# Performance work log

Measured on AMD Instinct MI355X. Metric: run time of the kernel, lower is better.

## Reference

```python
import jax, jax.numpy as jnp
import numpy as np

B, L, D = 4, 2048, 1024   # batch, seq_len, input_channels
S = 4096                  # param_token_num
DV = 1024                 # output_channels


def setup_inputs() -> dict:
    key = jax.random.key(0)
    k1, k2, k3 = jax.random.split(key, 3)
    return {
        "inputs": jax.random.normal(k1, (B, L, D), dtype=jnp.float32),
        "key_param_tokens": jax.random.normal(k2, (S, D), dtype=jnp.float32),
        "value_param_tokens": jax.random.normal(k3, (S, DV), dtype=jnp.float32),
    }


def reference(inputs, key_param_tokens, value_param_tokens):
    # scores: [B, L, S] — full score matrix (this is what a fused kernel would avoid)
    scores = jnp.einsum("bld,sd->bls", inputs, key_param_tokens)
    # gelu_l2_norm: exact (erf) gelu, then L2-normalize over S and rescale by sqrt(S)
    g = jax.nn.gelu(scores, approximate=False)
    l2 = jnp.linalg.norm(g, axis=-1, keepdims=True)
    w = g / l2 * jnp.sqrt(jnp.asarray(g.shape[-1], g.dtype))
    # weighted sum over param value tokens: [B, L, DV]
    return jnp.einsum("bls,sv->blv", w, value_param_tokens)
```

## Files before the change

### kernel.cpp

```cpp
#include <hip/hip_runtime.h>
#include <hip/hip_bf16.h>
#include <stdint.h>

#define M_ROWS 8192
#define D_DIM  1024
#define S_DIM  4096
#define DV_DIM 1024

typedef __attribute__((ext_vector_type(8))) short bf16x8;
typedef __attribute__((ext_vector_type(4))) float f32x4;
typedef unsigned short u16;

static __device__ __forceinline__ u16 f2bf(float x) {
  union { float f; unsigned u; } v; v.f = x;
  unsigned r = v.u + 0x7FFFu + ((v.u >> 16) & 1u);
  return (u16)(r >> 16);
}
static __device__ __forceinline__ float bf2f(u16 h) {
  union { unsigned u; float f; } v; v.u = ((unsigned)h) << 16;
  return v.f;
}
static __device__ __forceinline__ float gelu_fast(float x) {
  float u = 0.7978845608028654f * x * (1.0f + 0.044715f * x * x);
  float e = __expf(2.0f * u);
  float t = 1.0f - 2.0f / (e + 1.0f);
  return 0.5f * x * (1.0f + t);
}

static __device__ __forceinline__ void gload16(const void* g, void* l) {
  __builtin_amdgcn_global_load_lds(
      (__attribute__((address_space(1))) void*)(void*)(g),
      (__attribute__((address_space(3))) void*)(l), 16, 0, 0);
}

__global__ __launch_bounds__(256)
void cast_f32_bf16(const float* __restrict__ in, u16* __restrict__ out, int n4) {
  const int i = blockIdx.x * 256 + threadIdx.x;
  if (i >= n4) return;
  const float4 v = ((const float4*)in)[i];
  ushort4 o;
  o.x = f2bf(v.x); o.y = f2bf(v.y); o.z = f2bf(v.z); o.w = f2bf(v.w);
  ((ushort4*)out)[i] = o;
}

__global__ __launch_bounds__(256)
void transpose_cast(const float* __restrict__ V, u16* __restrict__ VT, int R, int C) {
  __shared__ float tile[32][33];
  const int tx = threadIdx.x & 31;
  const int ty = threadIdx.x >> 5;
  const int r0 = blockIdx.y * 32;
  const int c0 = blockIdx.x * 32;
#pragma unroll
  for (int dy = 0; dy < 32; dy += 8)
    tile[ty + dy][tx] = V[(long)(r0 + ty + dy) * C + (c0 + tx)];
  __syncthreads();
#pragma unroll
  for (int dy = 0; dy < 32; dy += 8)
    VT[(long)(c0 + ty + dy) * R + (r0 + tx)] = f2bf(tile[tx][ty + dy]);
}

__global__ __launch_bounds__(256)
void row_scale(const u16* __restrict__ G, float* __restrict__ scale, int S) {
  const int row = blockIdx.x;
  const u16* g = G + (long)row * S;
  float ssq = 0.f;
  for (int i = threadIdx.x * 8; i < S; i += 256 * 8) {
    bf16x8 v = *(const bf16x8*)&g[i];
#pragma unroll
    for (int j = 0; j < 8; ++j) {
      float f = bf2f((u16)v[j]);
      ssq += f * f;
    }
  }
#pragma unroll
  for (int off = 32; off > 0; off >>= 1)
    ssq += __shfl_down(ssq, off, 64);
  __shared__ float wsum[4];
  if ((threadIdx.x & 63) == 0) wsum[threadIdx.x >> 6] = ssq;
  __syncthreads();
  if (threadIdx.x == 0) {
    float t = wsum[0] + wsum[1] + wsum[2] + wsum[3];
    scale[row] = 64.0f * rsqrtf(t + 1e-30f);
  }
}

__global__ __launch_bounds__(256)
void add_inplace(float* __restrict__ Out, const float* __restrict__ P1, int n4) {
  for (int i = blockIdx.x * 256 + threadIdx.x; i < n4; i += 2048 * 256) {
    float4 a = ((const float4*)Out)[i];
    const float4 b = ((const float4*)P1)[i];
    a.x += b.x; a.y += b.y; a.z += b.z; a.w += b.w;
    ((float4*)Out)[i] = a;
  }
}


#define BARRIER asm volatile("s_barrier" ::: "memory")
#define VM4 asm volatile("s_waitcnt vmcnt(4)" ::: "memory")
#define VM2 asm volatile("s_waitcnt vmcnt(2)" ::: "memory")
#define VM0 asm volatile("s_waitcnt vmcnt(0)" ::: "memory")

#define PHASE(P, STAGES, WAITS)                                               \
  {                                                                           \
    bf16x8 af[2][2];                                                          \
    _Pragma("unroll")                                                         \
    for (int j = 0; j < 2; ++j) {                                             \
      const int ar = wm * 128 + ((P) * 2 + j) * 16 + fr;                      \
      af[j][0] = rdfrag(la, ar, 0);                                           \
      af[j][1] = rdfrag(la, ar, 1);                                           \
    }                                                                         \
    STAGES;                                                                   \
    BARRIER;                                                                  \
    __builtin_amdgcn_s_setprio(1);                                            \
    _Pragma("unroll")                                                         \
    for (int j = 0; j < 2; ++j) {                                             \
      _Pragma("unroll")                                                       \
      for (int n = 0; n < NF; ++n) {                                          \
        acc[(P) * 2 + j][n] = __builtin_amdgcn_mfma_f32_16x16x32_bf16(        \
            af[j][0], bfr[n][0], acc[(P) * 2 + j][n], 0, 0, 0);               \
        acc[(P) * 2 + j][n] = __builtin_amdgcn_mfma_f32_16x16x32_bf16(        \
            af[j][1], bfr[n][1], acc[(P) * 2 + j][n], 0, 0, 0);               \
      }                                                                       \
    }                                                                         \
    __builtin_amdgcn_s_setprio(0);                                            \
    WAITS;                                                                    \
    BARRIER;                                                                  \
  }

#define READ_B                                                                \
  {                                                                           \
    _Pragma("unroll")                                                         \
    for (int n = 0; n < NF; ++n) {                                            \
      const int br = wn * WNT + n * 16 + fr;                                  \
      bfr[n][0] = rdfrag(lb, br, 0);                                          \
      bfr[n][1] = rdfrag(lb, br, 1);                                          \
    }                                                                         \
  }

template <int MODE, int BN, bool SPLITK>
__global__ __launch_bounds__(512, 2)
void gemm8p(const u16* __restrict__ A, const u16* __restrict__ Bm,
            void* __restrict__ Cout0, void* __restrict__ Cout1,
            const float* __restrict__ scale,
            const int K, const int lda, const int ldb,
            const int N, const int nBN, const int nWG) {
  constexpr int BM = 256, BK = 64;
  constexpr int WNT = BN / 4;
  constexpr int NF = WNT / 16;

  __shared__ u16 ldsA[2][BM * BK];
  __shared__ u16 ldsB[2][BN * BK];

  const int tid = threadIdx.x;
  const int lane = tid & 63;
  const int wv = tid >> 6;
  const int wm = wv >> 2, wn = wv & 3;
  const int fr = lane & 15, hi = lane >> 4;

  int wg;
  {
    const int q = nWG >> 3, r = nWG & 7;
    const int x = blockIdx.x & 7, ix = blockIdx.x >> 3;
    wg = (x < r ? x * (q + 1) : r * (q + 1) + (x - r) * q) + ix;
  }
  void* Cout = Cout0;
  if constexpr (SPLITK) {
    const int half = nWG >> 1;
    const int ks = (wg >= half) ? 1 : 0;
    wg -= ks * half;
    A += (long)ks * K;
    Bm += (long)ks * K;
    if (ks) Cout = Cout1;
  }
  const int bm = wg / nBN, bn = wg % nBN;
  const long aR0 = (long)bm * BM;
  const long bR0 = (long)bn * BN;

  const int srow = tid >> 3;
  const int sch = (tid & 7) ^ (srow & 7);
  const long aoff = (aR0 + srow) * (long)lda + sch * 8;
  const long boff = (bR0 + srow) * (long)ldb + sch * 8;

  auto SA = [&](int buf, int r, int kOff) {
    gload16(A + aoff + ((long)r * 64) * lda + kOff, &ldsA[buf][r * 4096 + tid * 8]);
  };
  auto SB = [&](int buf, int r, int kOff) {
    gload16(Bm + boff + ((long)r * 64) * ldb + kOff, &ldsB[buf][r * 4096 + tid * 8]);
  };
  auto rdfrag = [&](const u16* base, int row, int kk) -> bf16x8 {
    return *(const bf16x8*)&base[row * 64 + (((kk << 2) | hi) ^ (row & 7)) * 8];
  };

  f32x4 acc[8][NF];
#pragma unroll
  for (int m = 0; m < 8; ++m)
#pragma unroll
    for (int n = 0; n < NF; ++n)
      acc[m][n] = f32x4{0.f, 0.f, 0.f, 0.f};

  bf16x8 bfr[NF][2];
  const int nK = K / BK;

  if constexpr (BN == 256) {
    SB(0, 0, 0); SB(0, 1, 0); SB(0, 2, 0); SB(0, 3, 0);
  } else {
    SB(0, 0, 0); SB(0, 1, 0);
  }
  SA(0, 0, 0); SA(0, 2, 0); SA(0, 1, 0); SA(0, 3, 0);
  VM2;
  BARRIER;

  int cur = 0;
  for (int kt = 0; kt < nK - 1; ++kt) {
    const int kN = (kt + 1) * BK;
    const int nxt = cur ^ 1;
    const u16* la = ldsA[cur];
    const u16* lb = ldsB[cur];
    READ_B;
    if constexpr (BN == 256) {
      PHASE(0, { SB(nxt, 0, kN); SB(nxt, 1, kN); }, {});
      PHASE(1, { SB(nxt, 2, kN); SB(nxt, 3, kN); }, VM4);
      PHASE(2, { SA(nxt, 0, kN); SA(nxt, 2, kN); }, {});
      PHASE(3, { SA(nxt, 1, kN); SA(nxt, 3, kN); }, VM2);
    } else {
      PHASE(0, { SB(nxt, 0, kN); SB(nxt, 1, kN); }, {});
      PHASE(1, { SA(nxt, 0, kN); SA(nxt, 2, kN); }, VM4);
      PHASE(2, { SA(nxt, 1, kN); SA(nxt, 3, kN); }, {});
      PHASE(3, {}, VM2);
    }
    cur ^= 1;
  }

  {
    const u16* la = ldsA[cur];
    const u16* lb = ldsB[cur];
    READ_B;
    PHASE(0, {}, {});
    PHASE(1, {}, VM0);
    PHASE(2, {}, {});
    PHASE(3, {}, {});
  }

  const long row0 = aR0 + wm * 128;
  const long col0 = bR0 + wn * WNT;
  if constexpr (MODE == 0) {
    u16* Cg = (u16*)Cout;
#pragma unroll
    for (int m = 0; m < 8; ++m) {
#pragma unroll
      for (int i = 0; i < 4; ++i) {
        const long r = row0 + m * 16 + hi * 4 + i;
#pragma unroll
        for (int n = 0; n < NF; ++n)
          Cg[r * N + col0 + n * 16 + fr] = f2bf(gelu_fast(acc[m][n][i]));
      }
    }
  } else {
    float* Cf = (float*)Cout;
#pragma unroll
    for (int m = 0; m < 8; ++m) {
#pragma unroll
      for (int i = 0; i < 4; ++i) {
        const long r = row0 + m * 16 + hi * 4 + i;
        const float s = scale[r];
#pragma unroll
        for (int n = 0; n < NF; ++n)
          Cf[r * N + col0 + n * 16 + fr] = acc[m][n][i] * s;
      }
    }
  }
}

extern "C" void kernel_launch(void* const* d_in, const int* in_sizes, int n_in,
                              void* d_out, int out_size, void* d_ws, size_t ws_size,
                              hipStream_t stream) {
  const float* Qf = (const float*)d_in[0];
  const float* Kf = (const float*)d_in[1];
  const float* Vf = (const float*)d_in[2];
  float* Out = (float*)d_out;

  const int M = M_ROWS, D = D_DIM, S = S_DIM, DV = DV_DIM;

  char* p = (char*)d_ws;
  u16* Qb = (u16*)p;            p += (size_t)M * D * 2;
  u16* Kb = (u16*)p;            p += (size_t)S * D * 2;
  u16* VT = (u16*)p;            p += (size_t)DV * S * 2;
  float* scalebuf = (float*)p;  p += (size_t)M * 4;
  u16* G = (u16*)p;
  const size_t fixed = (size_t)(p - (char*)d_ws);
  const size_t avail = (ws_size > fixed) ? (ws_size - fixed) : 0;

  const size_t bytes_per_row = (size_t)S * 2;
  size_t rows_fit = avail / bytes_per_row;
  int chunk = (int)((rows_fit / 256) * 256);
  if (chunk > M) chunk = M;
  if (chunk < 256) chunk = 256;

  const size_t Gbytes = (size_t)M * S * 2;
  const size_t Pbytes = (size_t)M * DV * 4;
  const bool use_split = (chunk >= M) && (avail >= Gbytes + Pbytes);
  float* P1 = (float*)((char*)G + Gbytes);

  cast_f32_bf16<<<(M * D / 4 + 255) / 256, 256, 0, stream>>>(Qf, Qb, M * D / 4);
  cast_f32_bf16<<<(S * D / 4 + 255) / 256, 256, 0, stream>>>(Kf, Kb, S * D / 4);
  transpose_cast<<<dim3(DV / 32, S / 32), 256, 0, stream>>>(Vf, VT, S, DV);

  const int nBN1 = S / 256;
  const int nBN2 = DV / 128;
  for (int m0 = 0; m0 < M; m0 += chunk) {
    const int rows = (M - m0 < chunk) ? (M - m0) : chunk;
    const int nWG1 = (rows / 256) * nBN1;
    gemm8p<0, 256, false><<<dim3(nWG1), 512, 0, stream>>>(
        Qb + (size_t)m0 * D, Kb, (void*)G, nullptr, nullptr, D, D, D, S, nBN1, nWG1);
    row_scale<<<rows, 256, 0, stream>>>(G, scalebuf, S);
    if (use_split) {
      const int nBNs = DV / 256;
      const int nWGs = 2 * (M / 256) * nBNs;
      gemm8p<1, 256, true><<<dim3(nWGs), 512, 0, stream>>>(
          G, VT, (void*)Out, (void*)P1, scalebuf, S / 2, S, S, DV, nBNs, nWGs);
      add_inplace<<<2048, 256, 0, stream>>>(Out, P1, M * DV / 4);
    } else {
      const int nWG2 = (rows / 256) * nBN2;
      gemm8p<1, 128, false><<<dim3(nWG2), 512, 0, stream>>>(
          G, VT, (void*)(Out + (size_t)m0 * DV), nullptr, scalebuf, S, S, S, DV, nBN2, nWG2);
    }
  }
}
```

Baseline: 191.0 us.

## Replace per-phase barriers with single end-of-iteration wait and barrier

Drops the barriers and partial vmcnt waits between the four MFMA phases of each K iteration. All next-tile global-to-LDS stages are issued up front, interleaved with the first clusters. A single vmcnt(0) wait plus one barrier then closes each iteration. The aim is to cut barrier overhead and let waves run out of step, at the cost of a coarser double-buffer schedule that exposes the full load latency at the end of each iteration.

```diff
diff --git a/kernel.cpp b/kernel.cpp
--- a/kernel.cpp
+++ b/kernel.cpp
@@ -96,11 +96,9 @@
 
 
 #define BARRIER asm volatile("s_barrier" ::: "memory")
-#define VM4 asm volatile("s_waitcnt vmcnt(4)" ::: "memory")
-#define VM2 asm volatile("s_waitcnt vmcnt(2)" ::: "memory")
 #define VM0 asm volatile("s_waitcnt vmcnt(0)" ::: "memory")
 
-#define PHASE(P, STAGES, WAITS)                                               \
+#define CLUSTER(P)                                                            \
   {                                                                           \
     bf16x8 af[2][2];                                                          \
     _Pragma("unroll")                                                         \
@@ -109,8 +107,6 @@
       af[j][0] = rdfrag(la, ar, 0);                                           \
       af[j][1] = rdfrag(la, ar, 1);                                           \
     }                                                                         \
-    STAGES;                                                                   \
-    BARRIER;                                                                  \
     __builtin_amdgcn_s_setprio(1);                                            \
     _Pragma("unroll")                                                         \
     for (int j = 0; j < 2; ++j) {                                             \
@@ -123,8 +119,6 @@
       }                                                                       \
     }                                                                         \
     __builtin_amdgcn_s_setprio(0);                                            \
-    WAITS;                                                                    \
-    BARRIER;                                                                  \
   }
 
 #define READ_B                                                                \
@@ -206,8 +200,8 @@
   } else {
     SB(0, 0, 0); SB(0, 1, 0);
   }
-  SA(0, 0, 0); SA(0, 2, 0); SA(0, 1, 0); SA(0, 3, 0);
-  VM2;
+  SA(0, 0, 0); SA(0, 1, 0); SA(0, 2, 0); SA(0, 3, 0);
+  VM0;
   BARRIER;
 
   int cur = 0;
@@ -218,16 +212,24 @@
     const u16* lb = ldsB[cur];
     READ_B;
     if constexpr (BN == 256) {
-      PHASE(0, { SB(nxt, 0, kN); SB(nxt, 1, kN); }, {});
-      PHASE(1, { SB(nxt, 2, kN); SB(nxt, 3, kN); }, VM4);
-      PHASE(2, { SA(nxt, 0, kN); SA(nxt, 2, kN); }, {});
-      PHASE(3, { SA(nxt, 1, kN); SA(nxt, 3, kN); }, VM2);
+      SB(nxt, 0, kN); SB(nxt, 1, kN); SB(nxt, 2, kN); SB(nxt, 3, kN);
+      SA(nxt, 0, kN); SA(nxt, 2, kN);
+      CLUSTER(0);
+      SA(nxt, 1, kN); SA(nxt, 3, kN);
+      CLUSTER(1);
+      CLUSTER(2);
+      CLUSTER(3);
     } else {
-      PHASE(0, { SB(nxt, 0, kN); SB(nxt, 1, kN); }, {});
-      PHASE(1, { SA(nxt, 0, kN); SA(nxt, 2, kN); }, VM4);
-      PHASE(2, { SA(nxt, 1, kN); SA(nxt, 3, kN); }, {});
-      PHASE(3, {}, VM2);
-    }
+      SB(nxt, 0, kN); SB(nxt, 1, kN);
+      SA(nxt, 0, kN); SA(nxt, 2, kN);
+      CLUSTER(0);
+      SA(nxt, 1, kN); SA(nxt, 3, kN);
+      CLUSTER(1);
+      CLUSTER(2);
+      CLUSTER(3);
+    }
+    VM0;
+    BARRIER;
     cur ^= 1;
   }
 
@@ -235,10 +237,10 @@
     const u16* la = ldsA[cur];
     const u16* lb = ldsB[cur];
     READ_B;
-    PHASE(0, {}, {});
-    PHASE(1, {}, VM0);
-    PHASE(2, {}, {});
-    PHASE(3, {}, {});
+    CLUSTER(0);
+    CLUSTER(1);
+    CLUSTER(2);
+    CLUSTER(3);
   }
 
   const long row0 = aR0 + wm * 128;
```

After: 211.1 us. 10.5% more time.

## Prefetch B tiles two stages ahead, issuing B loads into the current buffer after reads

Applied to the files above, without the earlier changes.

Restructures the GEMM main loop's global-to-LDS prefetch schedule. A is still loaded one K-step ahead, but B is now loaded two K-steps ahead, reusing the current B buffer after its fragments have been read into registers. This adds a peeled second-to-last iteration and changes the vmcnt waits. The aim is to hide global-load latency better. The risk is hazards from overwriting the current LDS buffer, plus more in-flight loads and different wait counts.

```diff
diff --git a/kernel.cpp b/kernel.cpp
--- a/kernel.cpp
+++ b/kernel.cpp
@@ -201,42 +201,58 @@
   bf16x8 bfr[NF][2];
   const int nK = K / BK;
 
+  SA(0, 0, 0); SA(0, 1, 0); SA(0, 2, 0); SA(0, 3, 0);
   if constexpr (BN == 256) {
     SB(0, 0, 0); SB(0, 1, 0); SB(0, 2, 0); SB(0, 3, 0);
+    SB(1, 0, BK); SB(1, 1, BK); SB(1, 2, BK); SB(1, 3, BK);
+    VM4;
   } else {
     SB(0, 0, 0); SB(0, 1, 0);
-  }
-  SA(0, 0, 0); SA(0, 2, 0); SA(0, 1, 0); SA(0, 3, 0);
-  VM2;
+    SB(1, 0, BK); SB(1, 1, BK);
+    VM2;
+  }
   BARRIER;
 
   int cur = 0;
-  for (int kt = 0; kt < nK - 1; ++kt) {
-    const int kN = (kt + 1) * BK;
+  for (int kt = 0; kt < nK - 2; ++kt) {
     const int nxt = cur ^ 1;
+    const int kA = (kt + 1) * BK;
+    const int kB = (kt + 2) * BK;
     const u16* la = ldsA[cur];
     const u16* lb = ldsB[cur];
     READ_B;
     if constexpr (BN == 256) {
-      PHASE(0, { SB(nxt, 0, kN); SB(nxt, 1, kN); }, {});
-      PHASE(1, { SB(nxt, 2, kN); SB(nxt, 3, kN); }, VM4);
-      PHASE(2, { SA(nxt, 0, kN); SA(nxt, 2, kN); }, {});
-      PHASE(3, { SA(nxt, 1, kN); SA(nxt, 3, kN); }, VM2);
+      PHASE(0, { SA(nxt, 0, kA); SA(nxt, 1, kA); SA(nxt, 2, kA); SA(nxt, 3, kA); }, {});
+      PHASE(1, { SB(cur, 0, kB); SB(cur, 1, kB); }, {});
+      PHASE(2, { SB(cur, 2, kB); SB(cur, 3, kB); }, {});
+      PHASE(3, {}, VM4);
     } else {
-      PHASE(0, { SB(nxt, 0, kN); SB(nxt, 1, kN); }, {});
-      PHASE(1, { SA(nxt, 0, kN); SA(nxt, 2, kN); }, VM4);
-      PHASE(2, { SA(nxt, 1, kN); SA(nxt, 3, kN); }, {});
+      PHASE(0, { SA(nxt, 0, kA); SA(nxt, 1, kA); SA(nxt, 2, kA); SA(nxt, 3, kA); }, {});
+      PHASE(1, { SB(cur, 0, kB); }, {});
+      PHASE(2, { SB(cur, 1, kB); }, {});
       PHASE(3, {}, VM2);
     }
     cur ^= 1;
   }
 
+  {
+    const int nxt = cur ^ 1;
+    const int kA = (nK - 1) * BK;
+    const u16* la = ldsA[cur];
+    const u16* lb = ldsB[cur];
+    READ_B;
+    PHASE(0, { SA(nxt, 0, kA); SA(nxt, 1, kA); SA(nxt, 2, kA); SA(nxt, 3, kA); }, {});
+    PHASE(1, {}, {});
+    PHASE(2, {}, {});
+    PHASE(3, {}, VM0);
+    cur ^= 1;
+  }
   {
     const u16* la = ldsA[cur];
     const u16* lb = ldsB[cur];
     READ_B;
     PHASE(0, {}, {});
-    PHASE(1, {}, VM0);
+    PHASE(1, {}, {});
     PHASE(2, {}, {});
     PHASE(3, {}, {});
   }
```

After: 203.9 us. 6.7% more time.

## Replace 8-wave GEMM with 4-wave kernel computing 128x128 per wave

Applied to the files above, without the earlier changes.

The bf16 MFMA GEMM now uses 256 threads (4 waves) per 256x256 tile instead of 512 threads (8 waves), and each wave computes a 128x128 sub-tile with an 8x8 accumulator array. Each wave therefore loads fewer LDS fragments per MFMA, and the staging of global-to-LDS copies and the vmcnt waits are reordered to fit the smaller wave count. The non-split second GEMM also switches from BN=128 to BN=256. In exchange, register pressure rises sharply (256 accumulator floats per lane) and occupancy falls to one block per CU with fewer waves to hide latency.

```diff
diff --git a/kernel.cpp b/kernel.cpp
--- a/kernel.cpp
+++ b/kernel.cpp
@@ -96,9 +96,7 @@
 
 
 #define BARRIER asm volatile("s_barrier" ::: "memory")
-#define VM4 asm volatile("s_waitcnt vmcnt(4)" ::: "memory")
-#define VM2 asm volatile("s_waitcnt vmcnt(2)" ::: "memory")
-#define VM0 asm volatile("s_waitcnt vmcnt(0)" ::: "memory")
+#define VMW(N) asm volatile("s_waitcnt vmcnt(" #N ")" ::: "memory")
 
 #define PHASE(P, STAGES, WAITS)                                               \
   {                                                                           \
@@ -115,7 +113,7 @@
     _Pragma("unroll")                                                         \
     for (int j = 0; j < 2; ++j) {                                             \
       _Pragma("unroll")                                                       \
-      for (int n = 0; n < NF; ++n) {                                          \
+      for (int n = 0; n < 8; ++n) {                                           \
         acc[(P) * 2 + j][n] = __builtin_amdgcn_mfma_f32_16x16x32_bf16(        \
             af[j][0], bfr[n][0], acc[(P) * 2 + j][n], 0, 0, 0);               \
         acc[(P) * 2 + j][n] = __builtin_amdgcn_mfma_f32_16x16x32_bf16(        \
@@ -130,23 +128,21 @@
 #define READ_B                                                                \
   {                                                                           \
     _Pragma("unroll")                                                         \
-    for (int n = 0; n < NF; ++n) {                                            \
-      const int br = wn * WNT + n * 16 + fr;                                  \
+    for (int n = 0; n < 8; ++n) {                                             \
+      const int br = wn * 128 + n * 16 + fr;                                  \
       bfr[n][0] = rdfrag(lb, br, 0);                                          \
       bfr[n][1] = rdfrag(lb, br, 1);                                          \
     }                                                                         \
   }
 
-template <int MODE, int BN, bool SPLITK>
-__global__ __launch_bounds__(512, 2)
-void gemm8p(const u16* __restrict__ A, const u16* __restrict__ Bm,
+template <int MODE, bool SPLITK>
+__global__ __launch_bounds__(256, 1)
+void gemm4f(const u16* __restrict__ A, const u16* __restrict__ Bm,
             void* __restrict__ Cout0, void* __restrict__ Cout1,
             const float* __restrict__ scale,
             const int K, const int lda, const int ldb,
             const int N, const int nBN, const int nWG) {
-  constexpr int BM = 256, BK = 64;
-  constexpr int WNT = BN / 4;
-  constexpr int NF = WNT / 16;
+  constexpr int BM = 256, BN = 256, BK = 64;
 
   __shared__ u16 ldsA[2][BM * BK];
   __shared__ u16 ldsB[2][BN * BK];
@@ -154,7 +150,7 @@
   const int tid = threadIdx.x;
   const int lane = tid & 63;
   const int wv = tid >> 6;
-  const int wm = wv >> 2, wn = wv & 3;
+  const int wm = wv >> 1, wn = wv & 1;
   const int fr = lane & 15, hi = lane >> 4;
 
   int wg;
@@ -182,32 +178,30 @@
   const long boff = (bR0 + srow) * (long)ldb + sch * 8;
 
   auto SA = [&](int buf, int r, int kOff) {
-    gload16(A + aoff + ((long)r * 64) * lda + kOff, &ldsA[buf][r * 4096 + tid * 8]);
+    gload16(A + aoff + ((long)r * 32) * lda + kOff, &ldsA[buf][r * 2048 + tid * 8]);
   };
   auto SB = [&](int buf, int r, int kOff) {
-    gload16(Bm + boff + ((long)r * 64) * ldb + kOff, &ldsB[buf][r * 4096 + tid * 8]);
+    gload16(Bm + boff + ((long)r * 32) * ldb + kOff, &ldsB[buf][r * 2048 + tid * 8]);
   };
   auto rdfrag = [&](const u16* base, int row, int kk) -> bf16x8 {
     return *(const bf16x8*)&base[row * 64 + (((kk << 2) | hi) ^ (row & 7)) * 8];
   };
 
-  f32x4 acc[8][NF];
+  f32x4 acc[8][8];
 #pragma unroll
   for (int m = 0; m < 8; ++m)
 #pragma unroll
-    for (int n = 0; n < NF; ++n)
+    for (int n = 0; n < 8; ++n)
       acc[m][n] = f32x4{0.f, 0.f, 0.f, 0.f};
 
-  bf16x8 bfr[NF][2];
+  bf16x8 bfr[8][2];
   const int nK = K / BK;
 
-  if constexpr (BN == 256) {
-    SB(0, 0, 0); SB(0, 1, 0); SB(0, 2, 0); SB(0, 3, 0);
-  } else {
-    SB(0, 0, 0); SB(0, 1, 0);
-  }
-  SA(0, 0, 0); SA(0, 2, 0); SA(0, 1, 0); SA(0, 3, 0);
-  VM2;
+  SB(0, 0, 0); SB(0, 1, 0); SB(0, 2, 0); SB(0, 3, 0);
+  SB(0, 4, 0); SB(0, 5, 0); SB(0, 6, 0); SB(0, 7, 0);
+  SA(0, 0, 0); SA(0, 4, 0); SA(0, 1, 0); SA(0, 5, 0);
+  SA(0, 2, 0); SA(0, 6, 0); SA(0, 3, 0); SA(0, 7, 0);
+  VMW(4);
   BARRIER;
 
   int cur = 0;
@@ -217,17 +211,10 @@
     const u16* la = ldsA[cur];
     const u16* lb = ldsB[cur];
     READ_B;
-    if constexpr (BN == 256) {
-      PHASE(0, { SB(nxt, 0, kN); SB(nxt, 1, kN); }, {});
-      PHASE(1, { SB(nxt, 2, kN); SB(nxt, 3, kN); }, VM4);
-      PHASE(2, { SA(nxt, 0, kN); SA(nxt, 2, kN); }, {});
-      PHASE(3, { SA(nxt, 1, kN); SA(nxt, 3, kN); }, VM2);
-    } else {
-      PHASE(0, { SB(nxt, 0, kN); SB(nxt, 1, kN); }, {});
-      PHASE(1, { SA(nxt, 0, kN); SA(nxt, 2, kN); }, VM4);
-      PHASE(2, { SA(nxt, 1, kN); SA(nxt, 3, kN); }, {});
-      PHASE(3, {}, VM2);
-    }
+    PHASE(0, { SB(nxt, 0, kN); SB(nxt, 1, kN); SB(nxt, 2, kN); SB(nxt, 3, kN); }, {});
+    PHASE(1, { SB(nxt, 4, kN); SB(nxt, 5, kN); SB(nxt, 6, kN); SB(nxt, 7, kN); }, VMW(10));
+    PHASE(2, { SA(nxt, 0, kN); SA(nxt, 4, kN); SA(nxt, 1, kN); SA(nxt, 5, kN); }, VMW(8));
+    PHASE(3, { SA(nxt, 2, kN); SA(nxt, 6, kN); SA(nxt, 3, kN); SA(nxt, 7, kN); }, VMW(4));
     cur ^= 1;
   }
 
@@ -236,13 +223,13 @@
     const u16* lb = ldsB[cur];
     READ_B;
     PHASE(0, {}, {});
-    PHASE(1, {}, VM0);
+    PHASE(1, {}, VMW(0));
     PHASE(2, {}, {});
     PHASE(3, {}, {});
   }
 
   const long row0 = aR0 + wm * 128;
-  const long col0 = bR0 + wn * WNT;
+  const long col0 = bR0 + wn * 128;
   if constexpr (MODE == 0) {
     u16* Cg = (u16*)Cout;
 #pragma unroll
@@ -251,7 +238,7 @@
       for (int i = 0; i < 4; ++i) {
         const long r = row0 + m * 16 + hi * 4 + i;
 #pragma unroll
-        for (int n = 0; n < NF; ++n)
+        for (int n = 0; n < 8; ++n)
           Cg[r * N + col0 + n * 16 + fr] = f2bf(gelu_fast(acc[m][n][i]));
       }
     }
@@ -264,7 +251,7 @@
         const long r = row0 + m * 16 + hi * 4 + i;
         const float s = scale[r];
 #pragma unroll
-        for (int n = 0; n < NF; ++n)
+        for (int n = 0; n < 8; ++n)
           Cf[r * N + col0 + n * 16 + fr] = acc[m][n][i] * s;
       }
     }
@@ -306,22 +293,21 @@
   transpose_cast<<<dim3(DV / 32, S / 32), 256, 0, stream>>>(Vf, VT, S, DV);
 
   const int nBN1 = S / 256;
-  const int nBN2 = DV / 128;
+  const int nBN2 = DV / 256;
   for (int m0 = 0; m0 < M; m0 += chunk) {
     const int rows = (M - m0 < chunk) ? (M - m0) : chunk;
     const int nWG1 = (rows / 256) * nBN1;
-    gemm8p<0, 256, false><<<dim3(nWG1), 512, 0, stream>>>(
+    gemm4f<0, false><<<dim3(nWG1), 256, 0, stream>>>(
         Qb + (size_t)m0 * D, Kb, (void*)G, nullptr, nullptr, D, D, D, S, nBN1, nWG1);
     row_scale<<<rows, 256, 0, stream>>>(G, scalebuf, S);
     if (use_split) {
-      const int nBNs = DV / 256;
-      const int nWGs = 2 * (M / 256) * nBNs;
-      gemm8p<1, 256, true><<<dim3(nWGs), 512, 0, stream>>>(
-          G, VT, (void*)Out, (void*)P1, scalebuf, S / 2, S, S, DV, nBNs, nWGs);
+      const int nWGs = 2 * (M / 256) * nBN2;
+      gemm4f<1, true><<<dim3(nWGs), 256, 0, stream>>>(
+          G, VT, (void*)Out, (void*)P1, scalebuf, S / 2, S, S, DV, nBN2, nWGs);
       add_inplace<<<2048, 256, 0, stream>>>(Out, P1, M * DV / 4);
     } else {
       const int nWG2 = (rows / 256) * nBN2;
-      gemm8p<1, 128, false><<<dim3(nWG2), 512, 0, stream>>>(
+      gemm4f<1, false><<<dim3(nWG2), 256, 0, stream>>>(
           G, VT, (void*)(Out + (size_t)m0 * DV), nullptr, scalebuf, S, S, S, DV, nBN2, nWG2);
     }
   }
```

Measured after the change: 206.0 us. +7.9%, slower.
